# Kernel optimization log

Hardware: AMD Instinct MI355X
Metric: run time of the kernel (lower is better)

The kernel has to match this reference:

```python
import jax, jax.numpy as jnp
import numpy as np

B, IN, H, F, T = 4096, 1024, 1024, 128, 3
LN_EPS = 1e-5


def setup_inputs() -> dict:
    key = jax.random.key(0)
    ks = jax.random.split(key, 12)
    inp = {
        "input_": jax.random.normal(ks[0], (B, IN), jnp.float32),
        "hx": jax.random.normal(ks[1], (B, H), jnp.float32),
        "cx": jax.random.normal(ks[2], (B, H), jnp.float32),
        "topic_w": jax.random.uniform(ks[3], (B, T), jnp.float32),
        # factorized gate weights (init scales per reset_parameters)
        "w_ih_a": jax.random.normal(ks[4], (4 * H, F), jnp.float32) / jnp.sqrt(F),
        "w_ih_b": jnp.full((F, T), 0.1 / T, jnp.float32),
        "w_ih_c": jax.random.normal(ks[5], (F, IN), jnp.float32) / jnp.sqrt(IN),
        "w_hh_a": 0.1 * jax.random.normal(ks[6], (4 * H, F), jnp.float32),
        "w_hh_b": jnp.full((F, T), 0.1 / T, jnp.float32),
        "w_hh_c": 0.1 * jax.random.normal(ks[7], (F, H), jnp.float32),
        # theta transforms: weight=0, bias=1 per reset_parameters
        "th_ih_w": jnp.zeros((T, T), jnp.float32),
        "th_ih_b": jnp.ones((T,), jnp.float32),
        "th_hh_w": jnp.zeros((T, T), jnp.float32),
        "th_hh_b": jnp.ones((T,), jnp.float32),
        # layernorm params
        "ln_i_w": jnp.ones((4 * H,), jnp.float32),
        "ln_i_b": jnp.zeros((4 * H,), jnp.float32),
        "ln_h_w": jnp.ones((4 * H,), jnp.float32),
        "ln_h_b": jnp.zeros((4 * H,), jnp.float32),
        "ln_c_w": jnp.ones((H,), jnp.float32),
        "ln_c_b": jnp.zeros((H,), jnp.float32),
    }
    return inp


def _ln(x, w, b):
    mu = x.mean(-1, keepdims=True)
    var = ((x - mu) ** 2).mean(-1, keepdims=True)
    return (x - mu) * jax.lax.rsqrt(var + LN_EPS) * w + b


def reference(input_, hx, cx, topic_w,
              w_ih_a, w_ih_b, w_ih_c, w_hh_a, w_hh_b, w_hh_c,
              th_ih_w, th_ih_b, th_hh_w, th_hh_b,
              ln_i_w, ln_i_b, ln_h_w, ln_h_b, ln_c_w, ln_c_b):
    # factorized input gates: ((x @ C^T) * (theta(topic) @ B^T)) @ A^T
    scale_i = (topic_w @ th_ih_w.T + th_ih_b) @ w_ih_b.T            # [B, F]
    igates = ((input_ @ w_ih_c.T) * scale_i) @ w_ih_a.T             # [B, 4H]
    scale_h = (topic_w @ th_hh_w.T + th_hh_b) @ w_hh_b.T            # [B, F]
    hgates = ((hx @ w_hh_c.T) * scale_h) @ w_hh_a.T                 # [B, 4H]

    gates = _ln(igates, ln_i_w, ln_i_b) + _ln(hgates, ln_h_w, ln_h_b)
    i, f, g, o = jnp.split(gates, 4, axis=1)
    i = jax.nn.sigmoid(i)
    f = jax.nn.sigmoid(f)
    g = jnp.tanh(g)  # dropout p=0 -> identity
    o = jax.nn.sigmoid(o)
    cy = _ln(f * cx + i * g, ln_c_w, ln_c_b)
    hy = o * jnp.tanh(cy)
    return hy, cy
```

## Files before the change

kernel.cpp:

```cpp
#include <hip/hip_runtime.h>

typedef unsigned short ushort_t;
typedef __attribute__((ext_vector_type(8))) short bf8_t;
typedef __attribute__((ext_vector_type(4))) float f4_t;

#define B_   4096
#define IN_  1024
#define H_   1024
#define F_   128
#define EPS_ 1e-5f

#define NG1   256
#define NPREP 256
#define NGRAM 128

#define NCH_  16
#define XSZ_  8192
#define LDSZ_ 40960

__device__ __forceinline__ float us2f(unsigned short s) {
  union { unsigned int u; float f; } v;
  v.u = ((unsigned int)s) << 16;
  return v.f;
}
__device__ __forceinline__ unsigned short f2us(float f) {
  union { float f; unsigned int u; } v;
  v.f = f;
  unsigned int r = (v.u + 0x7fffu + ((v.u >> 16) & 1u)) >> 16;
  return (unsigned short)r;
}
__device__ __forceinline__ float sigf(float x) { return 1.0f / (1.0f + __expf(-x)); }
__device__ __forceinline__ float tanh_f(float x) { return 1.0f - 2.0f / (1.0f + __expf(2.0f * x)); }

__device__ __forceinline__ int detect_fp32(const void* disc) {
  return ((const unsigned int*)disc)[0] == 0x3F800000u;
}
__device__ __forceinline__ float ldf(const void* p, int i, int fp32) {
  return fp32 ? ((const float*)p)[i] : us2f(((const ushort_t*)p)[i]);
}
__device__ __forceinline__ void ld8(const void* p, int idx, float* o, int fp32) {
  if (fp32) {
    const float4* q = (const float4*)((const float*)p + idx);
    float4 v0 = q[0], v1 = q[1];
    o[0]=v0.x; o[1]=v0.y; o[2]=v0.z; o[3]=v0.w;
    o[4]=v1.x; o[5]=v1.y; o[6]=v1.z; o[7]=v1.w;
  } else {
    uint4 v = *(const uint4*)((const ushort_t*)p + idx);
    const ushort_t* pv = (const ushort_t*)&v;
    #pragma unroll
    for (int i = 0; i < 8; i++) o[i] = us2f(pv[i]);
  }
}
__device__ __forceinline__ bf8_t cvt8p(const float* f) {
  union { bf8_t v; unsigned int u[4]; } r;
  const unsigned int* ui = (const unsigned int*)f;
  #pragma unroll
  for (int i = 0; i < 4; i++) {
    unsigned int lo = ui[2 * i] + 0x8000u;
    unsigned int hi = ui[2 * i + 1] + 0x8000u;
    r.u[i] = __builtin_amdgcn_perm(hi, lo, 0x07060302u);
  }
  return r.v;
}

__device__ __forceinline__ void gl_lds16(const void* g, void* l) {
  __builtin_amdgcn_global_load_lds(
      (const __attribute__((address_space(1))) unsigned int*)g,
      (__attribute__((address_space(3))) unsigned int*)l, 16, 0, 0);
}

__global__ __launch_bounds__(256, 4) void k_stageA(
    const void* __restrict__ X0, const void* __restrict__ X1,
    const void* __restrict__ Wc0, const void* __restrict__ Wc1,
    const void* __restrict__ Ai, const void* __restrict__ Ah,
    const void* __restrict__ lnwi, const void* __restrict__ lnwh,
    ushort_t* __restrict__ wb,
    float* __restrict__ cm_i, float* __restrict__ cm_h,
    float* __restrict__ g_i, float* __restrict__ g_h,
    float* __restrict__ C0, float* __restrict__ C1)
{
  __shared__ __align__(16) char lds_raw[LDSZ_];
  int bid = blockIdx.x, tid = threadIdx.x;
  int fp32 = detect_fp32(lnwi);

  if (bid < NG1) {
    int rb = bid >> 1, mat = bid & 1;
    const char* Xc = (const char*)(mat ? X1 : X0);
    const char* Wc = (const char*)(mat ? Wc1 : Wc0);
    float* C = mat ? C1 : C0;
    int lane = tid & 63, w = tid >> 6;
    int quad = lane >> 4, lcol = lane & 15;
    int brow0 = rb * 32;

    const char* srcp[10];
    #pragma unroll
    for (int j = 0; j < 10; j++) {
      int flat = (w * 10 + j) * 1024 + (lane << 4);
      if (flat < XSZ_) {
        int r = flat >> 8, inb = flat & 255;
        srcp[j] = Xc + (size_t)(brow0 + r) * 4096 + (inb ^ ((r & 7) << 5));
      } else {
        int fw = flat - XSZ_;
        int r = fw >> 8, inb = fw & 255;
        srcp[j] = Wc + (size_t)r * 4096 + (inb ^ ((r & 7) << 5));
      }
    }

    f4_t a00 = {0.f,0.f,0.f,0.f}, a01 = {0.f,0.f,0.f,0.f};
    f4_t a10 = {0.f,0.f,0.f,0.f}, a11 = {0.f,0.f,0.f,0.f};

    for (int kc0 = 0; kc0 < NCH_; kc0++) {
      int koff = kc0 * 256;
      #pragma unroll
      for (int j = 0; j < 10; j++)
        gl_lds16(srcp[j] + koff, lds_raw + (w * 10 + j) * 1024);
      __syncthreads();

      #pragma unroll
      for (int kc = 0; kc < 2; kc++) {
        int kb = kc * 128 + quad * 32;
        int kx = kb ^ ((lcol & 7) << 5);
        bf8_t af0, af1;
        {
          int ab = (0 * 16 + lcol) * 256 + kx;
          float4 v0 = *(const float4*)(lds_raw + ab);
          float4 v1 = *(const float4*)(lds_raw + ab + 16);
          float a8[8] = {v0.x, v0.y, v0.z, v0.w, v1.x, v1.y, v1.z, v1.w};
          af0 = cvt8p(a8);
        }
        {
          int ab = (1 * 16 + lcol) * 256 + kx;
          float4 v0 = *(const float4*)(lds_raw + ab);
          float4 v1 = *(const float4*)(lds_raw + ab + 16);
          float a8[8] = {v0.x, v0.y, v0.z, v0.w, v1.x, v1.y, v1.z, v1.w};
          af1 = cvt8p(a8);
        }
        #pragma unroll
        for (int t = 0; t < 2; t++) {
          int f = w * 32 + t * 16 + lcol;
          int wbyte = XSZ_ + f * 256 + kx;
          float4 b0 = *(const float4*)(lds_raw + wbyte);
          float4 b1 = *(const float4*)(lds_raw + wbyte + 16);
          float b8[8] = {b0.x, b0.y, b0.z, b0.w, b1.x, b1.y, b1.z, b1.w};
          bf8_t bf = cvt8p(b8);
          if (t == 0) {
            a00 = __builtin_amdgcn_mfma_f32_16x16x32_bf16(af0, bf, a00, 0, 0, 0);
            a10 = __builtin_amdgcn_mfma_f32_16x16x32_bf16(af1, bf, a10, 0, 0, 0);
          } else {
            a01 = __builtin_amdgcn_mfma_f32_16x16x32_bf16(af0, bf, a01, 0, 0, 0);
            a11 = __builtin_amdgcn_mfma_f32_16x16x32_bf16(af1, bf, a11, 0, 0, 0);
          }
        }
      }
      __syncthreads();
    }

    #pragma unroll
    for (int reg = 0; reg < 4; reg++) {
      int r0 = brow0 + quad * 4 + reg;
      C[r0 * F_ + w * 32 + lcol]            = a00[reg];
      C[r0 * F_ + w * 32 + 16 + lcol]       = a01[reg];
      C[(r0 + 16) * F_ + w * 32 + lcol]     = a10[reg];
      C[(r0 + 16) * F_ + w * 32 + 16 + lcol] = a11[reg];
    }
  } else if (bid < NG1 + NPREP) {
    int t = bid - NG1;
    #pragma unroll
    for (int i = 0; i < 16; i++) {
      int e = i * 256 + tid;
      int c = e >> 9, l = (e >> 3) & 63, j = e & 7;
      int k = c * 32 + ((l >> 4) << 3) + j;
      int n = t * 16 + (l & 15);
      float v;
      if (k < 128) v = ldf(Ai, n * F_ + k, fp32) * ldf(lnwi, n, fp32);
      else         v = ldf(Ah, n * F_ + (k - 128), fp32) * ldf(lnwh, n, fp32);
      wb[(size_t)t * 4096 + e] = f2us(v);
    }
    const void* A = (tid < 128) ? Ai : Ah;
    float* cm = (tid < 128) ? cm_i : cm_h;
    int f = tid & 127;
    float s = 0.f;
    #pragma unroll
    for (int i = 0; i < 16; i++) s += ldf(A, (t * 16 + i) * F_ + f, fp32);
    atomicAdd(&cm[f], s);
  } else {
    int g = bid - (NG1 + NPREP);
    int fblk = g & 3, mat = (g >> 2) & 1, z = g >> 3;
    const void* A = mat ? Ah : Ai;
    float* G = mat ? g_h : g_i;
    float (*As)[128] = (float(*)[128])lds_raw;
    int f1_0 = fblk * 32;
    int tf2 = tid & 31, tf1 = tid >> 5;
    float acc[4][4] = {};
    int nbase = z * 256;
    for (int n0 = nbase; n0 < nbase + 256; n0 += 32) {
      #pragma unroll
      for (int j = 0; j < 2; j++) {
        int idx = tid + 256 * j;
        int nn = idx >> 4, f8 = (idx & 15) * 8;
        float t[8];
        ld8(A, (n0 + nn) * F_ + f8, t, fp32);
        #pragma unroll
        for (int i = 0; i < 8; i++) As[nn][f8 + i] = t[i];
      }
      __syncthreads();
      #pragma unroll 4
      for (int nn = 0; nn < 32; nn++) {
        float4 a1 = *(const float4*)&As[nn][f1_0 + 4 * tf1];
        float4 a2 = *(const float4*)&As[nn][4 * tf2];
        const float* x1 = (const float*)&a1;
        const float* x2 = (const float*)&a2;
        #pragma unroll
        for (int i = 0; i < 4; i++)
          #pragma unroll
          for (int j = 0; j < 4; j++) acc[i][j] += x1[i] * x2[j];
      }
      __syncthreads();
    }
    #pragma unroll
    for (int i = 0; i < 4; i++)
      #pragma unroll
      for (int j = 0; j < 4; j++)
        atomicAdd(&G[(f1_0 + 4 * tf1 + i) * F_ + 4 * tf2 + j], acc[i][j]);
  }
}

__global__ __launch_bounds__(1024) void k_fused2(
    const float* __restrict__ C0g, const float* __restrict__ C1g,
    const float* __restrict__ g_i, const float* __restrict__ g_h,
    const float* __restrict__ cm_i, const float* __restrict__ cm_h,
    const void* __restrict__ topic,
    const void* __restrict__ thw0, const void* __restrict__ thw1,
    const void* __restrict__ thb0, const void* __restrict__ thb1,
    const void* __restrict__ wsb0, const void* __restrict__ wsb1,
    const ushort_t* __restrict__ wb,
    const void* __restrict__ lniw, const void* __restrict__ lnib,
    const void* __restrict__ lnhw, const void* __restrict__ lnhb,
    const void* __restrict__ lncw, const void* __restrict__ lncb,
    const void* __restrict__ cx, float* __restrict__ out)
{
  __shared__ float Cs[2][16][132];
  __shared__ __align__(16) ushort_t xs[4096];
  __shared__ float buf[16][1028];
  __shared__ float obuf[16][1028];
  __shared__ float p1part[2][4][16];
  __shared__ float p2s[2][16];
  __shared__ float rs2_s[2][16];
  __shared__ float mrs_s[2][16];
  __shared__ float wpart[16][16][2];
  __shared__ float mu_s[16], rs_s[16];

  int tid = threadIdx.x;
  int lane = tid & 63, w = tid >> 6;
  int quad = lane >> 4, lcol = lane & 15;
  int b0 = blockIdx.x * 16;
  int fp32 = detect_fp32(lniw);

  {
    int mat = tid >> 9, rem = tid & 511;
    int row = rem >> 5, f0 = (rem & 31) * 4;
    const float* C = mat ? C1g : C0g;
    const void* thw = mat ? thw1 : thw0;
    const void* thb = mat ? thb1 : thb0;
    const void* wbp = mat ? wsb1 : wsb0;
    float tp0 = ldf(topic, (b0 + row) * 3 + 0, fp32);
    float tp1 = ldf(topic, (b0 + row) * 3 + 1, fp32);
    float tp2 = ldf(topic, (b0 + row) * 3 + 2, fp32);
    float tv[3];
    #pragma unroll
    for (int t = 0; t < 3; t++)
      tv[t] = ldf(thb, t, fp32) + tp0 * ldf(thw, t * 3 + 0, fp32)
            + tp1 * ldf(thw, t * 3 + 1, fp32) + tp2 * ldf(thw, t * 3 + 2, fp32);
    float4 v = *(const float4*)&C[(size_t)(b0 + row) * F_ + f0];
    const float* vp = (const float*)&v;
    #pragma unroll
    for (int j = 0; j < 4; j++) {
      int f = f0 + j;
      float sc = tv[0] * ldf(wbp, f * 3 + 0, fp32)
               + tv[1] * ldf(wbp, f * 3 + 1, fp32)
               + tv[2] * ldf(wbp, f * 3 + 2, fp32);
      Cs[mat][row][f] = vp[j] * sc;
    }
  }
  __syncthreads();

  if (w < 8) {
    int w2 = w & 3, smat = w >> 2;
    const float* G  = smat ? g_h : g_i;
    const float* cm = smat ? cm_h : cm_i;
    bf8_t af[4];
    float p2p = 0.f;
    #pragma unroll
    for (int kc = 0; kc < 4; kc++) {
      int kb = kc * 32 + quad * 8;
      float a[8];
      #pragma unroll
      for (int j = 0; j < 8; j++) a[j] = Cs[smat][lcol][kb + j];
      af[kc] = cvt8p(a);
      if (w2 == 0) {
        #pragma unroll
        for (int j = 0; j < 8; j++) p2p += a[j] * cm[kb + j];
      }
    }
    float p1p[4] = {0.f, 0.f, 0.f, 0.f};
    #pragma unroll
    for (int t = 0; t < 2; t++) {
      int colf = (w2 * 2 + t) * 16 + lcol;
      f4_t acc = {0.f, 0.f, 0.f, 0.f};
      #pragma unroll
      for (int kc = 0; kc < 4; kc++) {
        const float4* qg = (const float4*)(G + colf * F_ + kc * 32 + quad * 8);
        float4 w0 = qg[0], w1 = qg[1];
        float bt[8] = {w0.x, w0.y, w0.z, w0.w, w1.x, w1.y, w1.z, w1.w};
        acc = __builtin_amdgcn_mfma_f32_16x16x32_bf16(af[kc], cvt8p(bt), acc, 0, 0, 0);
      }
      #pragma unroll
      for (int reg = 0; reg < 4; reg++)
        p1p[reg] += acc[reg] * Cs[smat][quad * 4 + reg][colf];
    }
    #pragma unroll
    for (int d = 1; d < 16; d <<= 1)
      #pragma unroll
      for (int reg = 0; reg < 4; reg++)
        p1p[reg] += __shfl_xor(p1p[reg], d, 64);
    if (lcol == 0) {
      #pragma unroll
      for (int reg = 0; reg < 4; reg++)
        p1part[smat][w2][quad * 4 + reg] = p1p[reg];
    }
    if (w2 == 0) {
      p2p += __shfl_xor(p2p, 16, 64);
      p2p += __shfl_xor(p2p, 32, 64);
      if (quad == 0) p2s[smat][lcol] = p2p;
    }
  }
  __syncthreads();
  if (tid < 32) {
    int m = tid >> 4, r = tid & 15;
    float p1 = p1part[m][0][r] + p1part[m][1][r] + p1part[m][2][r] + p1part[m][3][r];
    float E2 = p1 * (1.0f / 4096.0f);
    float mu = p2s[m][r] * (1.0f / 4096.0f);
    float rs = rsqrtf(E2 - mu * mu + EPS_);
    rs2_s[m][r] = rs;
    mrs_s[m][r] = mu * rs;
  }
  __syncthreads();

  if (tid < 512) {
    int m = tid >> 8, tt = tid & 255;
    int f = tt & 127, half = tt >> 7;
    int k = m * 128 + f;
    int c = k >> 5, lq = (k >> 3) & 3, j = k & 7;
    #pragma unroll
    for (int i = 0; i < 8; i++) {
      int r2 = half * 8 + i;
      int lfrag = r2 | (lq << 4);
      xs[c * 512 + lfrag * 8 + j] = f2us(Cs[m][r2][f] * rs2_s[m][r2]);
    }
  }
  __syncthreads();

  float mi[4], mh[4];
  #pragma unroll
  for (int reg = 0; reg < 4; reg++) {
    mi[reg] = mrs_s[0][quad * 4 + reg];
    mh[reg] = mrs_s[1][quad * 4 + reg];
  }

  float s1[4] = {0.f, 0.f, 0.f, 0.f}, s2[4] = {0.f, 0.f, 0.f, 0.f};

  #pragma unroll
  for (int q = 0; q < 4; q++) {
    int cg = w * 4 + q;
    int col = cg * 16 + lcol;
    float cxv[4];
    #pragma unroll
    for (int reg = 0; reg < 4; reg++)
      cxv[reg] = ldf(cx, (size_t)(b0 + quad * 4 + reg) * H_ + col, fp32);

    f4_t accg[4];
    #pragma unroll
    for (int g = 0; g < 4; g++) accg[g] = (f4_t){0.f, 0.f, 0.f, 0.f};
    #pragma unroll
    for (int c = 0; c < 8; c++) {
      bf8_t af = *(const bf8_t*)&xs[c * 512 + lane * 8];
      #pragma unroll
      for (int g = 0; g < 4; g++) {
        bf8_t bf = *(const bf8_t*)(wb + (size_t)(g * 64 + cg) * 4096 + c * 512 + lane * 8);
        accg[g] = __builtin_amdgcn_mfma_f32_16x16x32_bf16(af, bf, accg[g], 0, 0, 0);
      }
    }
    float liw0 = ldf(lniw, 0 * H_ + col, fp32), lib0 = ldf(lnib, 0 * H_ + col, fp32);
    float lhw0 = ldf(lnhw, 0 * H_ + col, fp32), lhb0 = ldf(lnhb, 0 * H_ + col, fp32);
    float liw1 = ldf(lniw, 1 * H_ + col, fp32), lib1 = ldf(lnib, 1 * H_ + col, fp32);
    float lhw1 = ldf(lnhw, 1 * H_ + col, fp32), lhb1 = ldf(lnhb, 1 * H_ + col, fp32);
    float liw2 = ldf(lniw, 2 * H_ + col, fp32), lib2 = ldf(lnib, 2 * H_ + col, fp32);
    float lhw2 = ldf(lnhw, 2 * H_ + col, fp32), lhb2 = ldf(lnhb, 2 * H_ + col, fp32);
    float liw3 = ldf(lniw, 3 * H_ + col, fp32), lib3 = ldf(lnib, 3 * H_ + col, fp32);
    float lhw3 = ldf(lnhw, 3 * H_ + col, fp32), lhb3 = ldf(lnhb, 3 * H_ + col, fp32);
    #pragma unroll
    for (int reg = 0; reg < 4; reg++) {
      int m = quad * 4 + reg;
      float gi = accg[0][reg] + lib0 + lhb0 - mi[reg] * liw0 - mh[reg] * lhw0;
      float gf = accg[1][reg] + lib1 + lhb1 - mi[reg] * liw1 - mh[reg] * lhw1;
      float gg = accg[2][reg] + lib2 + lhb2 - mi[reg] * liw2 - mh[reg] * lhw2;
      float go = accg[3][reg] + lib3 + lhb3 - mi[reg] * liw3 - mh[reg] * lhw3;
      float iv = sigf(gi), fv = sigf(gf), gv = tanh_f(gg), ov = sigf(go);
      float cval = fv * cxv[reg] + iv * gv;
      buf[m][col] = cval;
      obuf[m][col] = ov;
      s1[reg] += cval;
      s2[reg] += cval * cval;
    }
  }

  #pragma unroll
  for (int d = 1; d < 16; d <<= 1) {
    #pragma unroll
    for (int reg = 0; reg < 4; reg++) {
      s1[reg] += __shfl_xor(s1[reg], d, 64);
      s2[reg] += __shfl_xor(s2[reg], d, 64);
    }
  }
  if (lcol == 0) {
    #pragma unroll
    for (int reg = 0; reg < 4; reg++) {
      wpart[w][quad * 4 + reg][0] = s1[reg];
      wpart[w][quad * 4 + reg][1] = s2[reg];
    }
  }
  __syncthreads();
  if (tid < 16) {
    float t1 = 0.f, t2 = 0.f;
    #pragma unroll
    for (int ww = 0; ww < 16; ww++) { t1 += wpart[ww][tid][0]; t2 += wpart[ww][tid][1]; }
    float mu = t1 * (1.0f / 1024.0f);
    float var = t2 * (1.0f / 1024.0f) - mu * mu;
    mu_s[tid] = mu;
    rs_s[tid] = rsqrtf(var + EPS_);
  }
  __syncthreads();

  #pragma unroll
  for (int q = 0; q < 4; q++) {
    int col = (w * 4 + q) * 16 + lcol;
    float lw = ldf(lncw, col, fp32), lb = ldf(lncb, col, fp32);
    #pragma unroll
    for (int reg = 0; reg < 4; reg++) {
      int m = quad * 4 + reg;
      float cyv = (buf[m][col] - mu_s[m]) * rs_s[m] * lw + lb;
      out[(size_t)B_ * H_ + (size_t)(b0 + m) * H_ + col] = cyv;
      out[(size_t)(b0 + m) * H_ + col] = obuf[m][col] * tanh_f(cyv);
    }
  }
}

extern "C" void kernel_launch(void* const* d_in, const int* in_sizes, int n_in,
                              void* d_out, int out_size, void* d_ws, size_t ws_size,
                              hipStream_t stream) {
  const void* input_  = d_in[0];
  const void* hx      = d_in[1];
  const void* cx      = d_in[2];
  const void* topic   = d_in[3];
  const void* w_ih_a  = d_in[4];
  const void* w_ih_b  = d_in[5];
  const void* w_ih_c  = d_in[6];
  const void* w_hh_a  = d_in[7];
  const void* w_hh_b  = d_in[8];
  const void* w_hh_c  = d_in[9];
  const void* th_ih_w = d_in[10];
  const void* th_ih_b = d_in[11];
  const void* th_hh_w = d_in[12];
  const void* th_hh_b = d_in[13];
  const void* ln_i_w  = d_in[14];
  const void* ln_i_b  = d_in[15];
  const void* ln_h_w  = d_in[16];
  const void* ln_h_b  = d_in[17];
  const void* ln_c_w  = d_in[18];
  const void* ln_c_b  = d_in[19];

  float* w = (float*)d_ws;
  float* c1    = w;
  float* c2    = c1 + B_ * F_;
  float* g_i   = c2 + B_ * F_;
  float* g_h   = g_i + F_ * F_;
  float* cm_i  = g_h + F_ * F_;
  float* cm_h  = cm_i + F_;
  ushort_t* wbf = (ushort_t*)(cm_h + F_);

  hipMemsetAsync(g_i, 0, (size_t)(2 * F_ * F_ + 2 * F_) * sizeof(float), stream);

  k_stageA<<<dim3(NG1 + NPREP + NGRAM), dim3(256), 0, stream>>>(
      input_, hx, w_ih_c, w_hh_c,
      w_ih_a, w_hh_a, ln_i_w, ln_h_w,
      wbf, cm_i, cm_h, g_i, g_h, c1, c2);
  k_fused2<<<dim3(256), dim3(1024), 0, stream>>>(
      c1, c2, g_i, g_h, cm_i, cm_h,
      topic, th_ih_w, th_hh_w, th_ih_b, th_hh_b, w_ih_b, w_hh_b,
      wbf, ln_i_w, ln_i_b, ln_h_w, ln_h_b, ln_c_w, ln_c_b, cx, (float*)d_out);
}
```

Measured before the change: 200.3 us.

## Stage gate weights into LDS with async double-buffered loads in fused LSTM kernel

The second fused kernel used to read the bf16 gate weight fragments straight from global memory inside the MFMA loop. Now it stages them into a 128 KB LDS buffer with global-to-LDS copies, prefetching the next chunk while the current one is consumed. The per-row c and o staging buffers now reuse the same LDS region after the weights are finished. This aims to hide global load latency behind the MFMAs. In exchange it adds two block-wide barriers per chunk (64 in total) and uses a lot of LDS.

```diff
diff --git a/kernel.cpp b/kernel.cpp
--- a/kernel.cpp
+++ b/kernel.cpp
@@ -158,9 +158,9 @@
     #pragma unroll
     for (int reg = 0; reg < 4; reg++) {
       int r0 = brow0 + quad * 4 + reg;
-      C[r0 * F_ + w * 32 + lcol]            = a00[reg];
-      C[r0 * F_ + w * 32 + 16 + lcol]       = a01[reg];
-      C[(r0 + 16) * F_ + w * 32 + lcol]     = a10[reg];
+      C[r0 * F_ + w * 32 + lcol]             = a00[reg];
+      C[r0 * F_ + w * 32 + 16 + lcol]        = a01[reg];
+      C[(r0 + 16) * F_ + w * 32 + lcol]      = a10[reg];
       C[(r0 + 16) * F_ + w * 32 + 16 + lcol] = a11[reg];
     }
   } else if (bid < NG1 + NPREP) {
@@ -239,10 +239,9 @@
     const void* __restrict__ lncw, const void* __restrict__ lncb,
     const void* __restrict__ cx, float* __restrict__ out)
 {
+  __shared__ __align__(16) char wstage[131072];
   __shared__ float Cs[2][16][132];
   __shared__ __align__(16) ushort_t xs[4096];
-  __shared__ float buf[16][1028];
-  __shared__ float obuf[16][1028];
   __shared__ float p1part[2][4][16];
   __shared__ float p2s[2][16];
   __shared__ float rs2_s[2][16];
@@ -255,6 +254,18 @@
   int quad = lane >> 4, lcol = lane & 15;
   int b0 = blockIdx.x * 16;
   int fp32 = detect_fp32(lniw);
+
+#define STAGE_CHUNK(k) { \
+    char* Rr_ = wstage + (((k) >> 4) ? 65536 : 0); \
+    const ushort_t* srcT_ = wb \
+        + (size_t)((((k) >> 1) & 3) * 64 + 4 * w + ((k) >> 3)) * 4096 \
+        + ((k) & 1) * 2048 + lane * 8; \
+    _Pragma("unroll") \
+    for (int j_ = 0; j_ < 4; j_++) \
+      gl_lds16(srcT_ + j_ * 512, Rr_ + w * 4096 + j_ * 1024); \
+  }
+
+  STAGE_CHUNK(0);
 
   {
     int mat = tid >> 9, rem = tid & 511;
@@ -358,7 +369,6 @@
       xs[c * 512 + lfrag * 8 + j] = f2us(Cs[m][r2][f] * rs2_s[m][r2]);
     }
   }
-  __syncthreads();
 
   float mi[4], mh[4];
   #pragma unroll
@@ -370,49 +380,107 @@
   float s1[4] = {0.f, 0.f, 0.f, 0.f}, s2[4] = {0.f, 0.f, 0.f, 0.f};
 
   #pragma unroll
-  for (int q = 0; q < 4; q++) {
-    int cg = w * 4 + q;
-    int col = cg * 16 + lcol;
-    float cxv[4];
-    #pragma unroll
-    for (int reg = 0; reg < 4; reg++)
-      cxv[reg] = ldf(cx, (size_t)(b0 + quad * 4 + reg) * H_ + col, fp32);
-
-    f4_t accg[4];
-    #pragma unroll
-    for (int g = 0; g < 4; g++) accg[g] = (f4_t){0.f, 0.f, 0.f, 0.f};
-    #pragma unroll
-    for (int c = 0; c < 8; c++) {
-      bf8_t af = *(const bf8_t*)&xs[c * 512 + lane * 8];
+  for (int p = 0; p < 2; p++) {
+    float cv[2][4], ok[2][4];
+    #pragma unroll
+    for (int qq = 0; qq < 2; qq++) {
+      int q = 2 * p + qq;
+      int cg = w * 4 + q;
+      int col = cg * 16 + lcol;
+      float cxv[4];
+      #pragma unroll
+      for (int reg = 0; reg < 4; reg++)
+        cxv[reg] = ldf(cx, (b0 + quad * 4 + reg) * H_ + col, fp32);
+
+      f4_t gpre[4];
       #pragma unroll
       for (int g = 0; g < 4; g++) {
-        bf8_t bf = *(const bf8_t*)(wb + (size_t)(g * 64 + cg) * 4096 + c * 512 + lane * 8);
-        accg[g] = __builtin_amdgcn_mfma_f32_16x16x32_bf16(af, bf, accg[g], 0, 0, 0);
-      }
-    }
-    float liw0 = ldf(lniw, 0 * H_ + col, fp32), lib0 = ldf(lnib, 0 * H_ + col, fp32);
-    float lhw0 = ldf(lnhw, 0 * H_ + col, fp32), lhb0 = ldf(lnhb, 0 * H_ + col, fp32);
-    float liw1 = ldf(lniw, 1 * H_ + col, fp32), lib1 = ldf(lnib, 1 * H_ + col, fp32);
-    float lhw1 = ldf(lnhw, 1 * H_ + col, fp32), lhb1 = ldf(lnhb, 1 * H_ + col, fp32);
-    float liw2 = ldf(lniw, 2 * H_ + col, fp32), lib2 = ldf(lnib, 2 * H_ + col, fp32);
-    float lhw2 = ldf(lnhw, 2 * H_ + col, fp32), lhb2 = ldf(lnhb, 2 * H_ + col, fp32);
-    float liw3 = ldf(lniw, 3 * H_ + col, fp32), lib3 = ldf(lnib, 3 * H_ + col, fp32);
-    float lhw3 = ldf(lnhw, 3 * H_ + col, fp32), lhb3 = ldf(lnhb, 3 * H_ + col, fp32);
-    #pragma unroll
-    for (int reg = 0; reg < 4; reg++) {
-      int m = quad * 4 + reg;
-      float gi = accg[0][reg] + lib0 + lhb0 - mi[reg] * liw0 - mh[reg] * lhw0;
-      float gf = accg[1][reg] + lib1 + lhb1 - mi[reg] * liw1 - mh[reg] * lhw1;
-      float gg = accg[2][reg] + lib2 + lhb2 - mi[reg] * liw2 - mh[reg] * lhw2;
-      float go = accg[3][reg] + lib3 + lhb3 - mi[reg] * liw3 - mh[reg] * lhw3;
-      float iv = sigf(gi), fv = sigf(gf), gv = tanh_f(gg), ov = sigf(go);
-      float cval = fv * cxv[reg] + iv * gv;
-      buf[m][col] = cval;
-      obuf[m][col] = ov;
-      s1[reg] += cval;
-      s2[reg] += cval * cval;
-    }
-  }
+        f4_t acc = {0.f, 0.f, 0.f, 0.f};
+        #pragma unroll
+        for (int h = 0; h < 2; h++) {
+          int k = p * 16 + qq * 8 + g * 2 + h;
+          char* R = wstage + ((k >> 4) ? 65536 : 0);
+          __syncthreads();
+          #pragma unroll
+          for (int c4 = 0; c4 < 4; c4++) {
+            int c = h * 4 + c4;
+            bf8_t af = *(const bf8_t*)&xs[c * 512 + lane * 8];
+            bf8_t bf = *(const bf8_t*)(R + w * 4096 + c4 * 1024 + lane * 16);
+            acc = __builtin_amdgcn_mfma_f32_16x16x32_bf16(af, bf, acc, 0, 0, 0);
+          }
+          __syncthreads();
+          if (k == 0)  STAGE_CHUNK(1);
+          if (k == 1)  STAGE_CHUNK(2);
+          if (k == 2)  STAGE_CHUNK(3);
+          if (k == 3)  STAGE_CHUNK(4);
+          if (k == 4)  STAGE_CHUNK(5);
+          if (k == 5)  STAGE_CHUNK(6);
+          if (k == 6)  STAGE_CHUNK(7);
+          if (k == 7)  STAGE_CHUNK(8);
+          if (k == 8)  STAGE_CHUNK(9);
+          if (k == 9)  STAGE_CHUNK(10);
+          if (k == 10) STAGE_CHUNK(11);
+          if (k == 11) STAGE_CHUNK(12);
+          if (k == 12) STAGE_CHUNK(13);
+          if (k == 13) STAGE_CHUNK(14);
+          if (k == 14) STAGE_CHUNK(15);
+          if (k == 15) STAGE_CHUNK(16);
+          if (k == 16) STAGE_CHUNK(17);
+          if (k == 17) STAGE_CHUNK(18);
+          if (k == 18) STAGE_CHUNK(19);
+          if (k == 19) STAGE_CHUNK(20);
+          if (k == 20) STAGE_CHUNK(21);
+          if (k == 21) STAGE_CHUNK(22);
+          if (k == 22) STAGE_CHUNK(23);
+          if (k == 23) STAGE_CHUNK(24);
+          if (k == 24) STAGE_CHUNK(25);
+          if (k == 25) STAGE_CHUNK(26);
+          if (k == 26) STAGE_CHUNK(27);
+          if (k == 27) STAGE_CHUNK(28);
+          if (k == 28) STAGE_CHUNK(29);
+          if (k == 29) STAGE_CHUNK(30);
+          if (k == 30) STAGE_CHUNK(31);
+        }
+        gpre[g] = acc;
+      }
+
+      float liw0 = ldf(lniw, 0 * H_ + col, fp32), lib0 = ldf(lnib, 0 * H_ + col, fp32);
+      float lhw0 = ldf(lnhw, 0 * H_ + col, fp32), lhb0 = ldf(lnhb, 0 * H_ + col, fp32);
+      float liw1 = ldf(lniw, 1 * H_ + col, fp32), lib1 = ldf(lnib, 1 * H_ + col, fp32);
+      float lhw1 = ldf(lnhw, 1 * H_ + col, fp32), lhb1 = ldf(lnhb, 1 * H_ + col, fp32);
+      float liw2 = ldf(lniw, 2 * H_ + col, fp32), lib2 = ldf(lnib, 2 * H_ + col, fp32);
+      float lhw2 = ldf(lnhw, 2 * H_ + col, fp32), lhb2 = ldf(lnhb, 2 * H_ + col, fp32);
+      float liw3 = ldf(lniw, 3 * H_ + col, fp32), lib3 = ldf(lnib, 3 * H_ + col, fp32);
+      float lhw3 = ldf(lnhw, 3 * H_ + col, fp32), lhb3 = ldf(lnhb, 3 * H_ + col, fp32);
+      #pragma unroll
+      for (int reg = 0; reg < 4; reg++) {
+        float gi = gpre[0][reg] + lib0 + lhb0 - mi[reg] * liw0 - mh[reg] * lhw0;
+        float gf = gpre[1][reg] + lib1 + lhb1 - mi[reg] * liw1 - mh[reg] * lhw1;
+        float gg = gpre[2][reg] + lib2 + lhb2 - mi[reg] * liw2 - mh[reg] * lhw2;
+        float go = gpre[3][reg] + lib3 + lhb3 - mi[reg] * liw3 - mh[reg] * lhw3;
+        float iv = sigf(gi), fv = sigf(gf), gv = tanh_f(gg), ov = sigf(go);
+        float cval = fv * cxv[reg] + iv * gv;
+        cv[qq][reg] = cval;
+        ok[qq][reg] = ov;
+        s1[reg] += cval;
+        s2[reg] += cval * cval;
+      }
+    }
+    {
+      char* R = wstage + p * 65536;
+      #pragma unroll
+      for (int qq = 0; qq < 2; qq++) {
+        #pragma unroll
+        for (int reg = 0; reg < 4; reg++) {
+          int m = quad * 4 + reg;
+          int idx = m * 512 + w * 32 + qq * 16 + lcol;
+          *(float*)(R + idx * 4)         = cv[qq][reg];
+          *(float*)(R + 32768 + idx * 4) = ok[qq][reg];
+        }
+      }
+    }
+  }
+#undef STAGE_CHUNK
 
   #pragma unroll
   for (int d = 1; d < 16; d <<= 1) {
@@ -445,12 +513,17 @@
   for (int q = 0; q < 4; q++) {
     int col = (w * 4 + q) * 16 + lcol;
     float lw = ldf(lncw, col, fp32), lb = ldf(lncb, col, fp32);
+    const char* R = wstage + (q >> 1) * 65536;
+    int qq = q & 1;
     #pragma unroll
     for (int reg = 0; reg < 4; reg++) {
       int m = quad * 4 + reg;
-      float cyv = (buf[m][col] - mu_s[m]) * rs_s[m] * lw + lb;
+      int idx = m * 512 + w * 32 + qq * 16 + lcol;
+      float cval = *(const float*)(R + idx * 4);
+      float ov   = *(const float*)(R + 32768 + idx * 4);
+      float cyv = (cval - mu_s[m]) * rs_s[m] * lw + lb;
       out[(size_t)B_ * H_ + (size_t)(b0 + m) * H_ + col] = cyv;
-      out[(size_t)(b0 + m) * H_ + col] = obuf[m][col] * tanh_f(cyv);
+      out[(size_t)(b0 + m) * H_ + col] = ov * tanh_f(cyv);
     }
   }
 }
```

After: 224.6 us. +12.1%, slower.

## Double-buffer LDS chunks in stage-A factor GEMM to overlap loads with MFMA

Applied to the files above, without the earlier changes.

Doubles the stage-A LDS allocation to hold two K-chunks. Each iteration now issues the global-to-LDS loads for the next chunk before computing on the current one, replacing the two full __syncthreads per chunk with one barrier and explicit vmcnt waits. The goal is to hide global load latency behind MFMA work. In exchange, launch bounds drop from 4 to 2 blocks per CU, which reduces occupancy. The single barrier sits before the vmcnt wait, so waves may read LDS data that other waves have not finished loading, which is a possible race.

```diff
diff --git a/kernel.cpp b/kernel.cpp
--- a/kernel.cpp
+++ b/kernel.cpp
@@ -16,7 +16,8 @@
 
 #define NCH_  16
 #define XSZ_  8192
-#define LDSZ_ 40960
+#define CHSZ_ 40960
+#define LDSZ_ 81920
 
 __device__ __forceinline__ float us2f(unsigned short s) {
   union { unsigned int u; float f; } v;
@@ -69,7 +70,7 @@
       (__attribute__((address_space(3))) unsigned int*)l, 16, 0, 0);
 }
 
-__global__ __launch_bounds__(256, 4) void k_stageA(
+__global__ __launch_bounds__(256, 2) void k_stageA(
     const void* __restrict__ X0, const void* __restrict__ X1,
     const void* __restrict__ Wc0, const void* __restrict__ Wc1,
     const void* __restrict__ Ai, const void* __restrict__ Ah,
@@ -109,12 +110,27 @@
     f4_t a00 = {0.f,0.f,0.f,0.f}, a01 = {0.f,0.f,0.f,0.f};
     f4_t a10 = {0.f,0.f,0.f,0.f}, a11 = {0.f,0.f,0.f,0.f};
 
-    for (int kc0 = 0; kc0 < NCH_; kc0++) {
-      int koff = kc0 * 256;
-      #pragma unroll
-      for (int j = 0; j < 10; j++)
-        gl_lds16(srcp[j] + koff, lds_raw + (w * 10 + j) * 1024);
-      __syncthreads();
+#define STAGEC_(k, base) { \
+      int koff_ = (k) * 256; \
+      _Pragma("unroll") \
+      for (int j_ = 0; j_ < 10; j_++) \
+        gl_lds16(srcp[j_] + koff_, lds_raw + (base) + (w * 10 + j_) * 1024); \
+    }
+
+    STAGEC_(0, 0);
+
+    #pragma unroll
+    for (int k = 0; k < NCH_; k++) {
+      int base = (k & 1) ? CHSZ_ : 0;
+      __builtin_amdgcn_s_barrier();
+      if (k + 1 < NCH_) {
+        int nbase = ((k + 1) & 1) ? CHSZ_ : 0;
+        STAGEC_(k + 1, nbase);
+        asm volatile("s_waitcnt vmcnt(10)" ::: "memory");
+      } else {
+        asm volatile("s_waitcnt vmcnt(0)" ::: "memory");
+      }
+      __builtin_amdgcn_sched_barrier(0);
 
       #pragma unroll
       for (int kc = 0; kc < 2; kc++) {
@@ -122,14 +138,14 @@
         int kx = kb ^ ((lcol & 7) << 5);
         bf8_t af0, af1;
         {
-          int ab = (0 * 16 + lcol) * 256 + kx;
+          int ab = base + (0 * 16 + lcol) * 256 + kx;
           float4 v0 = *(const float4*)(lds_raw + ab);
           float4 v1 = *(const float4*)(lds_raw + ab + 16);
           float a8[8] = {v0.x, v0.y, v0.z, v0.w, v1.x, v1.y, v1.z, v1.w};
           af0 = cvt8p(a8);
         }
         {
-          int ab = (1 * 16 + lcol) * 256 + kx;
+          int ab = base + (1 * 16 + lcol) * 256 + kx;
           float4 v0 = *(const float4*)(lds_raw + ab);
           float4 v1 = *(const float4*)(lds_raw + ab + 16);
           float a8[8] = {v0.x, v0.y, v0.z, v0.w, v1.x, v1.y, v1.z, v1.w};
@@ -138,7 +154,7 @@
         #pragma unroll
         for (int t = 0; t < 2; t++) {
           int f = w * 32 + t * 16 + lcol;
-          int wbyte = XSZ_ + f * 256 + kx;
+          int wbyte = base + XSZ_ + f * 256 + kx;
           float4 b0 = *(const float4*)(lds_raw + wbyte);
           float4 b1 = *(const float4*)(lds_raw + wbyte + 16);
           float b8[8] = {b0.x, b0.y, b0.z, b0.w, b1.x, b1.y, b1.z, b1.w};
@@ -152,15 +168,15 @@
           }
         }
       }
-      __syncthreads();
-    }
+    }
+#undef STAGEC_
 
     #pragma unroll
     for (int reg = 0; reg < 4; reg++) {
       int r0 = brow0 + quad * 4 + reg;
-      C[r0 * F_ + w * 32 + lcol]            = a00[reg];
-      C[r0 * F_ + w * 32 + 16 + lcol]       = a01[reg];
-      C[(r0 + 16) * F_ + w * 32 + lcol]     = a10[reg];
+      C[r0 * F_ + w * 32 + lcol]             = a00[reg];
+      C[r0 * F_ + w * 32 + 16 + lcol]        = a01[reg];
+      C[(r0 + 16) * F_ + w * 32 + lcol]      = a10[reg];
       C[(r0 + 16) * F_ + w * 32 + 16 + lcol] = a11[reg];
     }
   } else if (bid < NG1 + NPREP) {
```

After: 201.4 us (median of 2 runs). Within noise of the previous version (+0.5%).
